# Kernel tuning notes

Hardware: AMD Instinct MI355X
Metric: run time of the kernel (lower is better)

Reference implementation:

```python
import jax, jax.numpy as jnp
import numpy as np

B, C, H, W = 8, 512, 64, 64
CR = C // 16  # reduced channels = 32


def setup_inputs() -> dict:
    key = jax.random.key(0)
    ks = jax.random.split(key, 10)
    s_in = 1.0 / np.sqrt(C)
    return {
        "x": jax.random.normal(ks[0], (B, C, H, W), jnp.float32),
        "Wq": jax.random.normal(ks[1], (CR, C), jnp.float32) * s_in,
        "bq": jnp.zeros((CR,), jnp.float32),
        "Wk": jax.random.normal(ks[2], (CR, C), jnp.float32) * s_in,
        "bk": jnp.zeros((CR,), jnp.float32),
        "Wv": jax.random.normal(ks[3], (C, C), jnp.float32) * s_in,
        "bv": jnp.zeros((C,), jnp.float32),
        "Wo": jax.random.normal(ks[4], (C, C), jnp.float32) * s_in,
        "bo": jnp.zeros((C,), jnp.float32),
        "gamma": jax.random.normal(ks[5], (1,), jnp.float32) * 0.1,
    }


def reference(x, Wq, bq, Wk, bk, Wv, bv, Wo, bo, gamma):
    b, c, h, w = x.shape
    n = h * w
    xf = x.reshape(b, c, n)  # [B,C,N]; 1x1 conv == channel matmul
    q = jnp.einsum('rc,bcn->bnr', Wq, xf) + bq  # [B,N,Cr]
    k = jnp.einsum('rc,bcn->brn', Wk, xf) + bk[None, :, None]  # [B,Cr,N]
    v = jnp.einsum('oc,bcn->bon', Wv, xf) + bv[None, :, None]  # [B,C,N]
    attn = jax.nn.softmax(jnp.einsum('bnr,brm->bnm', q, k), axis=-1)  # [B,N,N]
    out = jnp.einsum('bcm,bnm->bcn', v, attn)  # value @ attn^T -> [B,C,N]
    out = jnp.einsum('oc,bcn->bon', Wo, out) + bo[None, :, None]
    out = out.reshape(b, c, h, w)
    return gamma * out + x
```

## Files before the change

### kernel.cpp

```cpp
#include <hip/hip_runtime.h>
#include <stdint.h>

typedef unsigned short u16;
typedef float f32x4 __attribute__((ext_vector_type(4)));
typedef short short8 __attribute__((ext_vector_type(8)));

__device__ __forceinline__ u16 f2bf(float f) {
  union { float f; uint32_t u; } v; v.f = f;
  return (u16)((v.u + 0x7FFFu + ((v.u >> 16) & 1u)) >> 16);
}
__device__ __forceinline__ uint32_t pack2(u16 lo, u16 hi) {
  return (uint32_t)lo | ((uint32_t)hi << 16);
}
__device__ __forceinline__ void gld_lds16(const void* gsrc, void* ldst) {
  __builtin_amdgcn_global_load_lds(
      (const __attribute__((address_space(1))) unsigned int*)gsrc,
      (__attribute__((address_space(3))) unsigned int*)ldst, 16, 0, 0);
}

#define MFMA16(a, b, c) __builtin_amdgcn_mfma_f32_16x16x32_bf16((a), (b), (c), 0, 0, 0)

__global__ void conv_w(const float* __restrict__ src, u16* __restrict__ dst, int n4) {
  int i = blockIdx.x * blockDim.x + threadIdx.x;
  if (i >= n4) return;
  float4 v = ((const float4*)src)[i];
  uint2 p;
  p.x = pack2(f2bf(v.x), f2bf(v.y));
  p.y = pack2(f2bf(v.z), f2bf(v.w));
  ((uint2*)dst)[i] = p;
}

__global__ void conv_wqk(const float* __restrict__ Wq, const float* __restrict__ Wk,
                         u16* __restrict__ dst) {
  int i = blockIdx.x * blockDim.x + threadIdx.x;
  if (i >= 8192) return;
  const float LOG2E = 1.4426950408889634f;
  bool isQ = i < 4096;
  float4 v = isQ ? ((const float4*)Wq)[i] : ((const float4*)Wk)[i - 4096];
  float s = isQ ? LOG2E : 1.0f;
  uint2 p;
  p.x = pack2(f2bf(v.x * s), f2bf(v.y * s));
  p.y = pack2(f2bf(v.z * s), f2bf(v.w * s));
  ((uint2*)dst)[i] = p;
}

__global__ __launch_bounds__(256) void qkv_proj(
    const float* __restrict__ x, const u16* __restrict__ Wvb,
    const u16* __restrict__ Wqkb, const float* __restrict__ bv,
    const float* __restrict__ bq, const float* __restrict__ bk,
    u16* __restrict__ V2, u16* __restrict__ Qb, u16* __restrict__ Kb) {
  const int b = blockIdx.y, nb = blockIdx.x * 64;
  const int t = threadIdx.x, w = t >> 6, lane = t & 63, g = lane >> 4, l15 = lane & 15;
  const int wo = (w >> 1) * 32, wn = (w & 1) * 32;
  __shared__ __align__(16) u16 xT[64][64];

  f32x4 zero4 = {0.f, 0.f, 0.f, 0.f};
  f32x4 acc[8][2][2];
#pragma unroll
  for (int og = 0; og < 8; ++og)
#pragma unroll
    for (int ot = 0; ot < 2; ++ot)
#pragma unroll
      for (int nt = 0; nt < 2; ++nt) acc[og][ot][nt] = zero4;
  f32x4 accq[2][2];
  accq[0][0] = zero4; accq[0][1] = zero4; accq[1][0] = zero4; accq[1][1] = zero4;

  const int cq4 = (t >> 4) * 4, n4 = (t & 15) * 4;

  for (int c0 = 0; c0 < 512; c0 += 64) {
    float4 q0 = *(const float4*)&x[((size_t)(b * 512 + c0 + cq4 + 0)) * 4096 + nb + n4];
    float4 q1 = *(const float4*)&x[((size_t)(b * 512 + c0 + cq4 + 1)) * 4096 + nb + n4];
    float4 q2 = *(const float4*)&x[((size_t)(b * 512 + c0 + cq4 + 2)) * 4096 + nb + n4];
    float4 q3 = *(const float4*)&x[((size_t)(b * 512 + c0 + cq4 + 3)) * 4096 + nb + n4];
    float rr[4][4];
    rr[0][0] = q0.x; rr[0][1] = q0.y; rr[0][2] = q0.z; rr[0][3] = q0.w;
    rr[1][0] = q1.x; rr[1][1] = q1.y; rr[1][2] = q1.z; rr[1][3] = q1.w;
    rr[2][0] = q2.x; rr[2][1] = q2.y; rr[2][2] = q2.z; rr[2][3] = q2.w;
    rr[3][0] = q3.x; rr[3][1] = q3.y; rr[3][2] = q3.z; rr[3][3] = q3.w;
#pragma unroll
    for (int k = 0; k < 4; ++k) {
      int row = n4 + k;
      uint2 pk;
      pk.x = pack2(f2bf(rr[0][k]), f2bf(rr[1][k]));
      pk.y = pack2(f2bf(rr[2][k]), f2bf(rr[3][k]));
      int byte = row * 128 + ((cq4 * 2) ^ ((row & 7) << 4));
      *(uint2*)((char*)&xT[0][0] + byte) = pk;
    }
    __syncthreads();

    short8 bb[2][2];
#pragma unroll
    for (int nt = 0; nt < 2; ++nt)
#pragma unroll
      for (int ks = 0; ks < 2; ++ks) {
        int row = wn + nt * 16 + l15;
        int byte = row * 128 + (((ks * 64) + (g * 16)) ^ ((row & 7) << 4));
        bb[nt][ks] = *(const short8*)((const char*)&xT[0][0] + byte);
      }
#pragma unroll
    for (int og = 0; og < 8; ++og) {
      short8 af[2][2];
#pragma unroll
      for (int ot = 0; ot < 2; ++ot)
#pragma unroll
        for (int ks = 0; ks < 2; ++ks)
          af[ot][ks] = *(const short8*)&Wvb[(size_t)(og * 64 + wo + ot * 16 + l15) * 512 + c0 + ks * 32 + g * 8];
#pragma unroll
      for (int ks = 0; ks < 2; ++ks)
#pragma unroll
        for (int ot = 0; ot < 2; ++ot)
#pragma unroll
          for (int nt = 0; nt < 2; ++nt)
            acc[og][ot][nt] = MFMA16(af[ot][ks], bb[nt][ks], acc[og][ot][nt]);
    }
    {
      short8 aq[2][2];
#pragma unroll
      for (int ot = 0; ot < 2; ++ot)
#pragma unroll
        for (int ks = 0; ks < 2; ++ks)
          aq[ot][ks] = *(const short8*)&Wqkb[(size_t)(wo + ot * 16 + l15) * 512 + c0 + ks * 32 + g * 8];
#pragma unroll
      for (int ks = 0; ks < 2; ++ks)
#pragma unroll
        for (int ot = 0; ot < 2; ++ot)
#pragma unroll
          for (int nt = 0; nt < 2; ++nt)
            accq[ot][nt] = MFMA16(aq[ot][ks], bb[nt][ks], accq[ot][nt]);
    }
    __syncthreads();
  }

  const size_t tbase = (size_t)b * 2097152 + (size_t)(nb >> 6) * 32768;
#pragma unroll
  for (int og = 0; og < 8; ++og)
#pragma unroll
    for (int ot = 0; ot < 2; ++ot)
#pragma unroll
      for (int nt = 0; nt < 2; ++nt)
#pragma unroll
        for (int r = 0; r < 4; ++r) {
          int o = og * 64 + wo + ot * 16 + g * 4 + r;
          int kk = wn + nt * 16 + l15;
          int swz = ((kk * 2) ^ ((o & 7) << 4)) >> 1;
          V2[tbase + o * 64 + swz] = f2bf(acc[og][ot][nt][r] + bv[o]);
        }
  const float LOG2E = 1.4426950408889634f;
#pragma unroll
  for (int ot = 0; ot < 2; ++ot)
#pragma unroll
    for (int nt = 0; nt < 2; ++nt)
#pragma unroll
      for (int r = 0; r < 4; ++r) {
        int o = wo + ot * 16 + g * 4 + r;
        int n = nb + wn + nt * 16 + l15;
        if (o < 32) {
          Qb[((size_t)(b * 4096 + n)) * 32 + o] = f2bf(accq[ot][nt][r] + bq[o] * LOG2E);
        } else {
          Kb[((size_t)(b * 4096 + n)) * 32 + (o - 32)] = f2bf(accq[ot][nt][r] + bk[o - 32]);
        }
      }
}

__global__ __launch_bounds__(512, 1) void attn_f(
    const u16* __restrict__ Qb, const u16* __restrict__ Kb,
    const u16* __restrict__ V2, const u16* __restrict__ Wob,
    const float* __restrict__ bo, const float* __restrict__ gamma,
    const float* __restrict__ x, float* __restrict__ out) {
  const int bid = blockIdx.x;
  const int b = bid & 7;
  const int qblk = (bid >> 3) * 128;
  const int t = threadIdx.x;
  const int w = t >> 6, lane = t & 63, g = lane >> 4, l15 = lane & 15;
  const int qg = w & 3, chh = w >> 2;
  const int qbase = qblk + qg * 32;
  const int chb = chh * 256;

  __shared__ __align__(16) u16 Vlds[2][32768];
  __shared__ __align__(16) u16 Plds[4][32][88];
  __shared__ float lsum[4][32];

  f32x4 zero4 = {0.f, 0.f, 0.f, 0.f};

  short8 qf[2];
  if (chh == 0) {
#pragma unroll
    for (int qt = 0; qt < 2; ++qt)
      qf[qt] = *(const short8*)&Qb[((size_t)(b * 4096 + qbase + qt * 16 + l15)) * 32 + g * 8];
  }

  f32x4 acc[2][16];
#pragma unroll
  for (int qt = 0; qt < 2; ++qt)
#pragma unroll
    for (int ct = 0; ct < 16; ++ct) acc[qt][ct] = zero4;
  float l_[2][4] = {{0.f, 0.f, 0.f, 0.f}, {0.f, 0.f, 0.f, 0.f}};

  const char* VBb = (const char*)(V2 + (size_t)b * 2097152);
  const size_t kb0 = (size_t)b * 4096;

  {
    const char* gsrc = VBb + w * 8192 + lane * 16;
    char* ldst = (char*)&Vlds[0][0] + w * 8192;
#pragma unroll
    for (int j = 0; j < 8; ++j) gld_lds16(gsrc + j * 1024, ldst + j * 1024);
  }
  __syncthreads();

  for (int kv = 0; kv < 4096; kv += 64) {
    const int buf = (kv >> 6) & 1;
    const bool more = (kv + 64) < 4096;

    if (more) {
      const char* gsrc = VBb + (size_t)((kv >> 6) + 1) * 65536 + w * 8192 + lane * 16;
      char* ldst = (char*)&Vlds[buf ^ 1][0] + w * 8192;
#pragma unroll
      for (int j = 0; j < 8; ++j) gld_lds16(gsrc + j * 1024, ldst + j * 1024);
    }

    if (chh == 0) {
      f32x4 s[2][4];
#pragma unroll
      for (int ks = 0; ks < 4; ++ks) {
        short8 kf = *(const short8*)&Kb[(kb0 + kv + ks * 16 + l15) * 32 + g * 8];
        s[0][ks] = MFMA16(qf[0], kf, zero4);
        s[1][ks] = MFMA16(qf[1], kf, zero4);
      }
#pragma unroll
      for (int qt = 0; qt < 2; ++qt)
#pragma unroll
        for (int r = 0; r < 4; ++r) {
          float rs = 0.f;
#pragma unroll
          for (int ks = 0; ks < 4; ++ks) {
            float p = exp2f(s[qt][ks][r]);
            rs += p;
            Plds[qg][qt * 16 + g * 4 + r][ks * 16 + l15] = f2bf(p);
          }
          rs += __shfl_xor(rs, 1);
          rs += __shfl_xor(rs, 2);
          rs += __shfl_xor(rs, 4);
          rs += __shfl_xor(rs, 8);
          l_[qt][r] += rs;
        }
    }
    __syncthreads();

    short8 pf[2][2];
#pragma unroll
    for (int qt = 0; qt < 2; ++qt)
#pragma unroll
      for (int k2 = 0; k2 < 2; ++k2)
        pf[qt][k2] = *(const short8*)&Plds[qg][qt * 16 + l15][k2 * 32 + g * 8];
#pragma unroll
    for (int ct = 0; ct < 16; ++ct) {
      int c = chb + ct * 16 + l15;
      int sw = (c & 7) << 4;
      const char* vrow = (const char*)&Vlds[buf][0] + c * 128;
      short8 vf0 = *(const short8*)(vrow + ((g * 16) ^ sw));
      short8 vf1 = *(const short8*)(vrow + ((64 + g * 16) ^ sw));
      acc[0][ct] = MFMA16(pf[0][0], vf0, acc[0][ct]);
      acc[0][ct] = MFMA16(pf[0][1], vf1, acc[0][ct]);
      acc[1][ct] = MFMA16(pf[1][0], vf0, acc[1][ct]);
      acc[1][ct] = MFMA16(pf[1][1], vf1, acc[1][ct]);
    }
    __syncthreads();
  }

  if (chh == 0 && l15 == 0) {
#pragma unroll
    for (int qt = 0; qt < 2; ++qt)
#pragma unroll
      for (int r = 0; r < 4; ++r)
        lsum[qg][qt * 16 + g * 4 + r] = l_[qt][r];
  }
  __syncthreads();

  u16* AO = (u16*)&Vlds[0][0];
#pragma unroll
  for (int qt = 0; qt < 2; ++qt) {
    float inv[4];
#pragma unroll
    for (int r = 0; r < 4; ++r) inv[r] = 1.0f / lsum[qg][qt * 16 + g * 4 + r];
#pragma unroll
    for (int ct = 0; ct < 16; ++ct)
#pragma unroll
      for (int r = 0; r < 4; ++r) {
        int nrow = qg * 32 + qt * 16 + g * 4 + r;
        int c = chb + ct * 16 + l15;
        AO[nrow * 512 + (c ^ ((nrow & 7) << 3))] = f2bf(acc[qt][ct][r] * inv[r]);
      }
  }
  __syncthreads();

  f32x4 oacc[4][8];
#pragma unroll
  for (int ot = 0; ot < 4; ++ot)
#pragma unroll
    for (int nt = 0; nt < 8; ++nt) oacc[ot][nt] = zero4;

  for (int c0 = 0; c0 < 512; c0 += 64) {
#pragma unroll
    for (int nth = 0; nth < 2; ++nth) {
      short8 bb[4][2];
#pragma unroll
      for (int n2 = 0; n2 < 4; ++n2)
#pragma unroll
        for (int ks = 0; ks < 2; ++ks) {
          int row = (nth * 4 + n2) * 16 + l15;
          int coff = (c0 + ks * 32 + g * 8) ^ ((row & 7) << 3);
          bb[n2][ks] = *(const short8*)&AO[row * 512 + coff];
        }
#pragma unroll
      for (int ot = 0; ot < 4; ++ot) {
        short8 af[2];
#pragma unroll
        for (int ks = 0; ks < 2; ++ks)
          af[ks] = *(const short8*)&Wob[(size_t)(w * 64 + ot * 16 + l15) * 512 + c0 + ks * 32 + g * 8];
#pragma unroll
        for (int ks = 0; ks < 2; ++ks)
#pragma unroll
          for (int n2 = 0; n2 < 4; ++n2)
            oacc[ot][nth * 4 + n2] = MFMA16(af[ks], bb[n2][ks], oacc[ot][nth * 4 + n2]);
      }
    }
  }

  float gm = gamma[0];
#pragma unroll
  for (int ot = 0; ot < 4; ++ot)
#pragma unroll
    for (int nt = 0; nt < 8; ++nt)
#pragma unroll
      for (int r = 0; r < 4; ++r) {
        int o = w * 64 + ot * 16 + g * 4 + r;
        int n = qblk + nt * 16 + l15;
        size_t idx = ((size_t)(b * 512 + o)) * 4096 + n;
        out[idx] = gm * (oacc[ot][nt][r] + bo[o]) + x[idx];
      }
}

extern "C" void kernel_launch(void* const* d_in, const int* in_sizes, int n_in,
                              void* d_out, int out_size, void* d_ws, size_t ws_size,
                              hipStream_t stream) {
  (void)in_sizes; (void)n_in; (void)out_size; (void)ws_size;
  const float* x     = (const float*)d_in[0];
  const float* Wq    = (const float*)d_in[1];
  const float* bq    = (const float*)d_in[2];
  const float* Wk    = (const float*)d_in[3];
  const float* bk    = (const float*)d_in[4];
  const float* Wv    = (const float*)d_in[5];
  const float* bv    = (const float*)d_in[6];
  const float* Wo    = (const float*)d_in[7];
  const float* bo    = (const float*)d_in[8];
  const float* gamma = (const float*)d_in[9];

  char* wsb = (char*)d_ws;
  u16* V2   = (u16*)(wsb + 0);
  u16* Qb   = (u16*)(wsb + (size_t)33554432);
  u16* Kb   = (u16*)(wsb + (size_t)35651584);
  u16* Wvb  = (u16*)(wsb + (size_t)37748736);
  u16* Wob  = (u16*)(wsb + (size_t)38273024);
  u16* Wqkb = (u16*)(wsb + (size_t)38797312);

  conv_w<<<256, 256, 0, stream>>>(Wv, Wvb, 65536);
  conv_w<<<256, 256, 0, stream>>>(Wo, Wob, 65536);
  conv_wqk<<<32, 256, 0, stream>>>(Wq, Wk, Wqkb);
  qkv_proj<<<dim3(64, 8), 256, 0, stream>>>(x, Wvb, Wqkb, bv, bq, bk, V2, Qb, Kb);
  attn_f<<<256, 512, 0, stream>>>(Qb, Kb, V2, Wob, bo, gamma, x, (float*)d_out);
}
```

Baseline: 400.1 us.

## Software-pipeline QK^T softmax one KV tile ahead of PV MFMAs

```diff
diff --git a/kernel.cpp b/kernel.cpp
--- a/kernel.cpp
+++ b/kernel.cpp
@@ -205,7 +205,41 @@
 #pragma unroll
     for (int j = 0; j < 8; ++j) gld_lds16(gsrc + j * 1024, ldst + j * 1024);
   }
-  __syncthreads();
+  if (chh == 0) {
+    float rsv[2][4];
+#pragma unroll
+    for (int half = 0; half < 2; ++half) {
+      short8 kfA = *(const short8*)&Kb[(kb0 + 0 + half * 32 + 0 + l15) * 32 + g * 8];
+      short8 kfB = *(const short8*)&Kb[(kb0 + 0 + half * 32 + 16 + l15) * 32 + g * 8];
+      f32x4 sA[2], sB[2];
+      sA[0] = MFMA16(qf[0], kfA, zero4); sA[1] = MFMA16(qf[1], kfA, zero4);
+      sB[0] = MFMA16(qf[0], kfB, zero4); sB[1] = MFMA16(qf[1], kfB, zero4);
+#pragma unroll
+      for (int qt = 0; qt < 2; ++qt)
+#pragma unroll
+        for (int r = 0; r < 4; ++r) {
+          float pA = exp2f(sA[qt][r]), pB = exp2f(sB[qt][r]);
+          Plds[qg][qt * 16 + g * 4 + r][(half * 2 + 0) * 16 + l15] = f2bf(pA);
+          Plds[qg][qt * 16 + g * 4 + r][(half * 2 + 1) * 16 + l15] = f2bf(pB);
+          float v = pA + pB;
+          rsv[qt][r] = half ? (rsv[qt][r] + v) : v;
+        }
+    }
+#pragma unroll
+    for (int qt = 0; qt < 2; ++qt)
+#pragma unroll
+      for (int r = 0; r < 4; ++r) {
+        float rs = rsv[qt][r];
+        rs += __shfl_xor(rs, 1);
+        rs += __shfl_xor(rs, 2);
+        rs += __shfl_xor(rs, 4);
+        rs += __shfl_xor(rs, 8);
+        l_[qt][r] += rs;
+      }
+  }
+  asm volatile("s_waitcnt vmcnt(0) lgkmcnt(0)" ::: "memory");
+  __builtin_amdgcn_s_barrier();
+  __builtin_amdgcn_sched_barrier(0);
 
   for (int kv = 0; kv < 4096; kv += 64) {
     const int buf = (kv >> 6) & 1;
@@ -218,25 +252,42 @@
       for (int j = 0; j < 8; ++j) gld_lds16(gsrc + j * 1024, ldst + j * 1024);
     }
 
-    if (chh == 0) {
-      f32x4 s[2][4];
-#pragma unroll
-      for (int ks = 0; ks < 4; ++ks) {
-        short8 kf = *(const short8*)&Kb[(kb0 + kv + ks * 16 + l15) * 32 + g * 8];
-        s[0][ks] = MFMA16(qf[0], kf, zero4);
-        s[1][ks] = MFMA16(qf[1], kf, zero4);
+    short8 pf[2][2];
+#pragma unroll
+    for (int qt = 0; qt < 2; ++qt)
+#pragma unroll
+      for (int k2 = 0; k2 < 2; ++k2)
+        pf[qt][k2] = *(const short8*)&Plds[qg][qt * 16 + l15][k2 * 32 + g * 8];
+
+    asm volatile("s_waitcnt lgkmcnt(0)" ::: "memory");
+    __builtin_amdgcn_s_barrier();
+    __builtin_amdgcn_sched_barrier(0);
+
+    if (chh == 0 && more) {
+      float rsv[2][4];
+#pragma unroll
+      for (int half = 0; half < 2; ++half) {
+        short8 kfA = *(const short8*)&Kb[(kb0 + kv + 64 + half * 32 + 0 + l15) * 32 + g * 8];
+        short8 kfB = *(const short8*)&Kb[(kb0 + kv + 64 + half * 32 + 16 + l15) * 32 + g * 8];
+        f32x4 sA[2], sB[2];
+        sA[0] = MFMA16(qf[0], kfA, zero4); sA[1] = MFMA16(qf[1], kfA, zero4);
+        sB[0] = MFMA16(qf[0], kfB, zero4); sB[1] = MFMA16(qf[1], kfB, zero4);
+#pragma unroll
+        for (int qt = 0; qt < 2; ++qt)
+#pragma unroll
+          for (int r = 0; r < 4; ++r) {
+            float pA = exp2f(sA[qt][r]), pB = exp2f(sB[qt][r]);
+            Plds[qg][qt * 16 + g * 4 + r][(half * 2 + 0) * 16 + l15] = f2bf(pA);
+            Plds[qg][qt * 16 + g * 4 + r][(half * 2 + 1) * 16 + l15] = f2bf(pB);
+            float v = pA + pB;
+            rsv[qt][r] = half ? (rsv[qt][r] + v) : v;
+          }
       }
 #pragma unroll
       for (int qt = 0; qt < 2; ++qt)
 #pragma unroll
         for (int r = 0; r < 4; ++r) {
-          float rs = 0.f;
-#pragma unroll
-          for (int ks = 0; ks < 4; ++ks) {
-            float p = exp2f(s[qt][ks][r]);
-            rs += p;
-            Plds[qg][qt * 16 + g * 4 + r][ks * 16 + l15] = f2bf(p);
-          }
+          float rs = rsv[qt][r];
           rs += __shfl_xor(rs, 1);
           rs += __shfl_xor(rs, 2);
           rs += __shfl_xor(rs, 4);
@@ -244,14 +295,7 @@
           l_[qt][r] += rs;
         }
     }
-    __syncthreads();
-
-    short8 pf[2][2];
-#pragma unroll
-    for (int qt = 0; qt < 2; ++qt)
-#pragma unroll
-      for (int k2 = 0; k2 < 2; ++k2)
-        pf[qt][k2] = *(const short8*)&Plds[qg][qt * 16 + l15][k2 * 32 + g * 8];
+
 #pragma unroll
     for (int ct = 0; ct < 16; ++ct) {
       int c = chb + ct * 16 + l15;
@@ -264,7 +308,10 @@
       acc[1][ct] = MFMA16(pf[1][0], vf0, acc[1][ct]);
       acc[1][ct] = MFMA16(pf[1][1], vf1, acc[1][ct]);
     }
-    __syncthreads();
+
+    asm volatile("s_waitcnt vmcnt(0) lgkmcnt(0)" ::: "memory");
+    __builtin_amdgcn_s_barrier();
+    __builtin_amdgcn_sched_barrier(0);
   }
 
   if (chh == 0 && l15 == 0) {
```

Result: faster. 387.8 us (-3.1%).
